# Performance work log

Measured on AMD Instinct MI355X. Metric: run time of the kernel, lower is better.

## Reference

```python
import jax, jax.numpy as jnp
import numpy as np

D_MODEL = 256; N_HEADS = 8; N_LEVELS = 4; N_POINTS = 4
D_HEAD = D_MODEL // N_HEADS


def setup_inputs() -> dict:
    key = jax.random.key(0)
    ks = jax.random.split(key, 8)
    N, Lq = 4, 4096
    shapes = np.array([4096, 2048, 1024, 512], dtype=np.int32)  # temporal lengths per level
    Len_in = int(shapes.sum())  # 7680
    start = np.concatenate([[0], np.cumsum(shapes)[:-1]]).astype(np.int32)
    HLP = N_HEADS * N_LEVELS * N_POINTS
    return {
        "query": jax.random.normal(ks[0], (N, Lq, D_MODEL), jnp.float32),
        "reference_points": jax.random.uniform(ks[1], (N, Lq, N_LEVELS, 1), jnp.float32),
        "input_flatten": jax.random.normal(ks[2], (N, Len_in, D_MODEL), jnp.float32),
        "input_spatial_shapes": jnp.asarray(shapes),
        "input_level_start_index": jnp.asarray(start),
        "W_off": jax.random.normal(ks[3], (D_MODEL, HLP), jnp.float32) * 0.01,
        "b_off": jax.random.normal(ks[4], (HLP,), jnp.float32) * 2.0,
        "W_aw": jax.random.normal(ks[5], (D_MODEL, HLP), jnp.float32) * 0.02,
        "b_aw": jnp.zeros((HLP,), jnp.float32),
        "W_v": jax.random.normal(ks[6], (D_MODEL, D_MODEL), jnp.float32) / np.sqrt(D_MODEL).astype(np.float32),
        "b_v": jnp.zeros((D_MODEL,), jnp.float32),
        "W_out": jax.random.normal(ks[7], (D_MODEL, D_MODEL), jnp.float32) / np.sqrt(D_MODEL).astype(np.float32),
        "b_out": jnp.zeros((D_MODEL,), jnp.float32),
    }


def reference(query, reference_points, input_flatten, input_spatial_shapes,
              input_level_start_index, W_off, b_off, W_aw, b_aw, W_v, b_v,
              W_out, b_out):
    N, Lq, C = query.shape
    M, L, P, Dh = N_HEADS, N_LEVELS, N_POINTS, D_HEAD
    S = input_flatten.shape[1]

    value = (input_flatten @ W_v + b_v).reshape(N, S, M, Dh)
    off = (query @ W_off + b_off).reshape(N, Lq, M, L, P)
    aw = jax.nn.softmax((query @ W_aw + b_aw).reshape(N, Lq, M, L * P), axis=-1)
    aw = aw.reshape(N, Lq, M, L, P)

    # reference_points last dim == 1 branch: loc = ref + off / T_l, in [0,1]
    T = input_spatial_shapes.astype(jnp.float32)[None, None, None, :, None]  # [1,1,1,L,1]
    loc = reference_points[:, :, None, :, None, 0] + off / T  # [N,Lq,M,L,P]

    # grid_sample(align_corners=False, padding_mode='border') along W with H=1, y=0.5:
    # pixel coord x = loc*T - 0.5, clamped to [0, T-1], then linear interp.
    x = jnp.clip(loc * T - 0.5, 0.0, T - 1.0)
    x0 = jnp.floor(x)
    w1 = x - x0                                   # frac weight for right neighbor
    i0 = x0.astype(jnp.int32)
    i1 = jnp.minimum(i0 + 1, input_spatial_shapes[None, None, None, :, None] - 1)
    base = input_level_start_index[None, None, None, :, None]
    g0 = i0 + base                                # global flattened indices [N,Lq,M,L,P]
    g1 = i1 + base

    v = value.transpose(0, 2, 1, 3)               # [N,M,S,Dh]

    def gather(idx):
        idxt = idx.transpose(0, 2, 1, 3, 4).reshape(N, M, Lq * L * P, 1)
        return jnp.take_along_axis(v, idxt, axis=2).reshape(N, M, Lq, L, P, Dh)

    s0 = gather(g0)
    s1 = gather(g1)
    w1t = w1.transpose(0, 2, 1, 3, 4)[..., None]   # [N,M,Lq,L,P,1]
    samp = s0 * (1.0 - w1t) + s1 * w1t             # [N,M,Lq,L,P,Dh]

    awt = aw.transpose(0, 2, 1, 3, 4)[..., None]
    out = (samp * awt).sum(axis=(3, 4))            # [N,M,Lq,Dh]
    out = out.transpose(0, 2, 1, 3).reshape(N, Lq, M * Dh)
    return out @ W_out + b_out
```

## Files before the change

kernel.cpp:

```cpp
#include <hip/hip_runtime.h>
#include <hip/hip_bf16.h>
#include <cstddef>
#include <cstdint>

#define D_MODEL   256
#define N_HEADS   8
#define N_LEVELS  4
#define N_POINTS  4
#define D_HEAD    32
#define HLP       128
#define NBATCH    4
#define LQ        4096
#define S_LEN     7680

typedef __attribute__((ext_vector_type(8))) short  short8;
typedef __attribute__((ext_vector_type(4))) float  f32x4;
typedef __attribute__((ext_vector_type(4))) int    i32x4;
typedef __attribute__((ext_vector_type(8))) unsigned short ushort8;

__device__ __forceinline__ unsigned short f2bf(float x) {
    __hip_bfloat16 h = __float2bfloat16(x);
    return *reinterpret_cast<unsigned short*>(&h);
}
__device__ __forceinline__ float bf2f(unsigned short u) {
    unsigned int v = ((unsigned int)u) << 16;
    return *reinterpret_cast<float*>(&v);
}

__device__ __forceinline__ void gload_lds16(const void* g, void* l) {
    __builtin_amdgcn_global_load_lds(
        (const __attribute__((address_space(1))) void*)g,
        (__attribute__((address_space(3))) void*)l,
        16, 0, 0);
}

__global__ __launch_bounds__(256) void prep_kernel(
    const float* __restrict__ W_v,  const float* __restrict__ W_off,
    const float* __restrict__ W_aw, const float* __restrict__ W_out,
    const float* __restrict__ b_off, const float* __restrict__ b_aw,
    unsigned short* __restrict__ Wv_t, unsigned short* __restrict__ Wcat_t,
    unsigned short* __restrict__ Wout_t, float* __restrict__ bcat)
{
    __shared__ float t[64][65];
    const int z   = blockIdx.z;
    const int k0  = blockIdx.y * 64;
    const int n0  = blockIdx.x * 64;
    const int tid = threadIdx.x;

    const float* src; int srcN; int cs; unsigned short* dst;
    if (z == 0)      { src = W_v;   srcN = 256; cs = n0;       dst = Wv_t;  }
    else if (z == 2) { src = W_out; srcN = 256; cs = n0;       dst = Wout_t;}
    else if (n0 < 128){ src = W_off; srcN = 128; cs = n0;      dst = Wcat_t;}
    else             { src = W_aw;  srcN = 128; cs = n0 - 128; dst = Wcat_t;}

    #pragma unroll
    for (int i = 0; i < 16; ++i) {
        int idx = tid + i * 256;
        int kk = idx >> 6, nn = idx & 63;
        t[kk][nn] = src[(size_t)(k0 + kk) * srcN + cs + nn];
    }
    __syncthreads();
    #pragma unroll
    for (int i = 0; i < 16; ++i) {
        int idx = tid + i * 256;
        int nn = idx >> 6, kk = idx & 63;
        dst[(size_t)(n0 + nn) * 256 + k0 + kk] = f2bf(t[kk][nn]);
    }
    if (z == 1 && blockIdx.x == 0 && blockIdx.y == 0) {
        bcat[tid] = (tid < 128) ? b_off[tid] : b_aw[tid - 128];
    }
}

__global__ __launch_bounds__(256) void gemm_vp_kernel(
    const float* __restrict__ inflat, const float* __restrict__ query,
    const unsigned short* __restrict__ Wv_t, const unsigned short* __restrict__ Wcat_t,
    const float* __restrict__ b_v, const float* __restrict__ bcat,
    unsigned short* __restrict__ value3, float* __restrict__ P)
{
    __shared__ alignas(16) unsigned short Abuf[2][4][64][8];
    __shared__ alignas(16) unsigned short Bbuf[2][8][64][8];

    const int job = blockIdx.x;
    const bool is_val = (job < 960);
    const int jj   = is_val ? job : (job - 960);
    const int row0 = (jj >> 1) * 64;
    const int col0 = (jj & 1) * 128;
    const float* A = is_val ? inflat : query;
    const unsigned short* Bt = is_val ? Wv_t : Wcat_t;
    const float* bias = is_val ? b_v : bcat;

    const int tid  = threadIdx.x;
    const int lane = tid & 63;
    const int w    = tid >> 6;
    const int lr   = lane & 15;
    const int lk   = (lane >> 4) * 8;

    const int ar = tid >> 2;
    const int ak = (tid & 3) * 8;
    const int afrag = ar >> 4;
    const int alane = ((ak >> 3) << 4) | (ar & 15);
    const float* Arow = A + (size_t)(row0 + ar) * 256 + ak;
    const unsigned short* Bcol = Bt + (size_t)(col0 + lr) * 256 + lk;

    f32x4 acc[8] = {};

    float4 pa0 = *(const float4*)(Arow);
    float4 pa1 = *(const float4*)(Arow + 4);
    #pragma unroll
    for (int c = 0; c < 2; ++c) {
        const int in = w * 2 + c;
        gload_lds16(Bcol + (size_t)in * 16 * 256, &Bbuf[0][in][0][0]);
    }

    for (int kt = 0; kt < 8; ++kt) {
        const int cur = kt & 1;
        short8 pk;
        pk[0] = (short)f2bf(pa0.x); pk[1] = (short)f2bf(pa0.y);
        pk[2] = (short)f2bf(pa0.z); pk[3] = (short)f2bf(pa0.w);
        pk[4] = (short)f2bf(pa1.x); pk[5] = (short)f2bf(pa1.y);
        pk[6] = (short)f2bf(pa1.z); pk[7] = (short)f2bf(pa1.w);
        *(short8*)&Abuf[cur][afrag][alane][0] = pk;
        __syncthreads();

        if (kt < 7) {
            const int k1 = (kt + 1) * 32;
            pa0 = *(const float4*)(Arow + k1);
            pa1 = *(const float4*)(Arow + k1 + 4);
            #pragma unroll
            for (int c = 0; c < 2; ++c) {
                const int in = w * 2 + c;
                gload_lds16(Bcol + (size_t)in * 16 * 256 + k1, &Bbuf[1 - cur][in][0][0]);
            }
        }

        const short8 af = *(const short8*)&Abuf[cur][w][lane][0];
        #pragma unroll
        for (int j = 0; j < 8; ++j) {
            const short8 bf = *(const short8*)&Bbuf[cur][j][lane][0];
            acc[j] = __builtin_amdgcn_mfma_f32_16x16x32_bf16(af, bf, acc[j], 0, 0, 0);
        }
    }

    const int prow = (lane >> 4) * 4;
    const int pcol = lane & 15;
    const int rbase = row0 + w * 16 + prow;
    if (is_val) {
        const int n  = row0 / S_LEN;
        const int s0 = row0 - n * S_LEN + w * 16 + prow;
        #pragma unroll
        for (int j = 0; j < 8; ++j) {
            const int col = col0 + j * 16 + pcol;
            const float bs = bias[col];
            const int m = col >> 5, d = col & 31;
            unsigned short* dst = value3 + ((size_t)(n * 8 + m) * S_LEN + s0) * 32 + d;
            #pragma unroll
            for (int r = 0; r < 4; ++r)
                dst[(size_t)r * 32] = f2bf(acc[j][r] + bs);
        }
    } else {
        #pragma unroll
        for (int j = 0; j < 8; ++j) {
            const int col = col0 + j * 16 + pcol;
            const float bs = bias[col];
            #pragma unroll
            for (int r = 0; r < 4; ++r)
                P[(size_t)(rbase + r) * 256 + col] = acc[j][r] + bs;
        }
    }
}

__global__ __launch_bounds__(512, 4) void sample_out_kernel(
    const float* __restrict__ P, const float* __restrict__ refp,
    const int* __restrict__ shapes, const int* __restrict__ lstart,
    const unsigned short* __restrict__ value3,
    const unsigned short* __restrict__ Wout_t,
    const float* __restrict__ b_out,
    float* __restrict__ Cout)
{
    __shared__ alignas(16) unsigned short t_lds[16][264];

    const int b    = blockIdx.x;
    const int xcd  = b & 7;
    const int n    = xcd >> 1;
    const int half = xcd & 1;
    const int slot = b >> 3;
    const int q0   = (slot * 2 + half) * 16;
    const int nq0  = n * LQ + q0;
    const int tid  = threadIdx.x;

    {
        const int q   = tid >> 5;
        const int sub = tid & 31;
        const int m   = sub >> 2;
        const int ql  = sub & 3;
        const int nq  = nq0 + q;

        const i32x4 sh4 = *(const i32x4*)shapes;
        const i32x4 ls4 = *(const i32x4*)lstart;
        const f32x4 rf4 = *(const f32x4*)(refp + (size_t)nq * N_LEVELS);

        float e[16], wgt[16];
        int   g0a[16], glim[4];
        #pragma unroll
        for (int l = 0; l < 4; ++l) {
            const f32x4 off = __builtin_nontemporal_load(
                (const f32x4*)(P + (size_t)nq * 256 + m * 16 + l * 4));
            const f32x4 lg  = __builtin_nontemporal_load(
                (const f32x4*)(P + (size_t)nq * 256 + 128 + m * 16 + l * 4));
            const float Tf = (float)sh4[l];
            glim[l] = ls4[l] + sh4[l] - 1;
            #pragma unroll
            for (int k = 0; k < 4; ++k) {
                float x = rf4[l] * Tf + off[k] - 0.5f;
                x = fminf(fmaxf(x, 0.0f), Tf - 1.0f);
                const float x0 = floorf(x);
                g0a[l * 4 + k] = (int)x0 + ls4[l];
                wgt[l * 4 + k] = x - x0;
                e  [l * 4 + k] = lg[k];
            }
        }

        float mx = -1e30f;
        #pragma unroll
        for (int i = 0; i < 16; ++i) mx = fmaxf(mx, e[i]);
        float s = 0.f;
        #pragma unroll
        for (int i = 0; i < 16; ++i) { e[i] = __expf(e[i] - mx); s += e[i]; }
        const float rs = 1.0f / s;

        const unsigned short* vb =
            value3 + (size_t)(n * 8 + m) * S_LEN * 32 + ql * 8;

        float acc[8] = {};
        #pragma unroll
        for (int i = 0; i < 16; ++i) {
            const float a  = e[i] * rs;
            const float ww = wgt[i];
            const int g0 = g0a[i];
            const int g1 = min(g0 + 1, glim[i >> 2]);
            const ushort8 u0 = *(const ushort8*)(vb + (size_t)g0 * 32);
            const ushort8 u1 = *(const ushort8*)(vb + (size_t)g1 * 32);
            #pragma unroll
            for (int d = 0; d < 8; ++d) {
                const float v0 = bf2f(u0[d]);
                const float v1 = bf2f(u1[d]);
                acc[d] += a * (v0 + ww * (v1 - v0));
            }
        }
        ushort8 o;
        #pragma unroll
        for (int d = 0; d < 8; ++d) o[d] = f2bf(acc[d]);
        *(ushort8*)&t_lds[q][m * 32 + ql * 8] = o;
    }
    __syncthreads();

    const int lane = tid & 63;
    const int wv   = tid >> 6;
    const int arow = lane & 15;
    const int kgrp = (lane >> 4) * 8;
    const int n0   = wv * 32;

    short8 af[8];
    #pragma unroll
    for (int kt = 0; kt < 8; ++kt)
        af[kt] = *(const short8*)&t_lds[arow][kt * 32 + kgrp];

    f32x4 oacc[2] = {};
    #pragma unroll
    for (int j = 0; j < 2; ++j) {
        const unsigned short* bp =
            Wout_t + (size_t)(n0 + j * 16 + arow) * 256 + kgrp;
        #pragma unroll
        for (int kt = 0; kt < 8; ++kt) {
            const short8 bf = *(const short8*)(bp + kt * 32);
            oacc[j] = __builtin_amdgcn_mfma_f32_16x16x32_bf16(af[kt], bf, oacc[j], 0, 0, 0);
        }
    }

    const int prow = (lane >> 4) * 4;
    const int pcol = lane & 15;
    #pragma unroll
    for (int j = 0; j < 2; ++j) {
        const int col = n0 + j * 16 + pcol;
        const float bs = b_out[col];
        #pragma unroll
        for (int r = 0; r < 4; ++r)
            __builtin_nontemporal_store(oacc[j][r] + bs,
                Cout + (size_t)(nq0 + prow + r) * 256 + col);
    }
}

extern "C" void kernel_launch(void* const* d_in, const int* in_sizes, int n_in,
                              void* d_out, int out_size, void* d_ws, size_t ws_size,
                              hipStream_t stream)
{
    const float* query  = (const float*)d_in[0];
    const float* refp   = (const float*)d_in[1];
    const float* inflat = (const float*)d_in[2];
    const int*   shapes = (const int*)d_in[3];
    const int*   lstart = (const int*)d_in[4];
    const float* W_off  = (const float*)d_in[5];
    const float* b_off  = (const float*)d_in[6];
    const float* W_aw   = (const float*)d_in[7];
    const float* b_aw   = (const float*)d_in[8];
    const float* W_v    = (const float*)d_in[9];
    const float* b_v    = (const float*)d_in[10];
    const float* W_out  = (const float*)d_in[11];
    const float* b_out  = (const float*)d_in[12];

    const int M_val = NBATCH * S_LEN;
    const int M_q   = NBATCH * LQ;

    char* p = (char*)d_ws;
    unsigned short* value3 = (unsigned short*)p; p += (size_t)M_val * D_MODEL * 2;
    float*          P      = (float*)p;          p += (size_t)M_q * 256 * 4;
    unsigned short* Wv_t   = (unsigned short*)p; p += 256 * 256 * 2;
    unsigned short* Wcat_t = (unsigned short*)p; p += 256 * 256 * 2;
    unsigned short* Wout_t = (unsigned short*)p; p += 256 * 256 * 2;
    float*          bcat   = (float*)p;          p += 256 * 4;

    prep_kernel<<<dim3(4, 4, 3), 256, 0, stream>>>(
        W_v, W_off, W_aw, W_out, b_off, b_aw, Wv_t, Wcat_t, Wout_t, bcat);
    gemm_vp_kernel<<<1472, 256, 0, stream>>>(
        inflat, query, Wv_t, Wcat_t, b_v, bcat, value3, P);
    sample_out_kernel<<<1024, 512, 0, stream>>>(
        P, refp, shapes, lstart, value3, Wout_t, b_out, (float*)d_out);
}
```

Measured before the change: 168.5 us.

## Split sampling levels across two lanes and halve queries per block

Each thread now samples only two of the four levels for its head slice, and partial sums from the paired lane are combined with a cross-lane shuffle. Blocks handle 8 queries instead of 16 and the grid is doubled, raising parallelism and in-flight gathers. The output GEMM still runs on 16 rows, half of them unused, so MFMA work and W_out loads per useful row double.

```diff
diff --git a/kernel.cpp b/kernel.cpp
--- a/kernel.cpp
+++ b/kernel.cpp
@@ -17,6 +17,7 @@
 typedef __attribute__((ext_vector_type(4))) float  f32x4;
 typedef __attribute__((ext_vector_type(4))) int    i32x4;
 typedef __attribute__((ext_vector_type(8))) unsigned short ushort8;
+typedef __attribute__((ext_vector_type(4))) unsigned short ushortv4;
 
 __device__ __forceinline__ unsigned short f2bf(float x) {
     __hip_bfloat16 h = __float2bfloat16(x);
@@ -184,39 +185,45 @@
     const int n    = xcd >> 1;
     const int half = xcd & 1;
     const int slot = b >> 3;
-    const int q0   = (slot * 2 + half) * 16;
+    const int q0   = (slot * 2 + half) * 8;
     const int nq0  = n * LQ + q0;
     const int tid  = threadIdx.x;
+    const int lane = tid & 63;
 
     {
-        const int q   = tid >> 5;
-        const int sub = tid & 31;
-        const int m   = sub >> 2;
-        const int ql  = sub & 3;
-        const int nq  = nq0 + q;
+        const int q  = tid >> 6;
+        const int m  = lane >> 3;
+        const int h  = (lane >> 2) & 1;
+        const int ql = lane & 3;
+        const int nq = nq0 + q;
 
         const i32x4 sh4 = *(const i32x4*)shapes;
         const i32x4 ls4 = *(const i32x4*)lstart;
         const f32x4 rf4 = *(const f32x4*)(refp + (size_t)nq * N_LEVELS);
 
-        float e[16], wgt[16];
-        int   g0a[16], glim[4];
+        float e[16];
         #pragma unroll
         for (int l = 0; l < 4; ++l) {
+            const f32x4 lg = __builtin_nontemporal_load(
+                (const f32x4*)(P + (size_t)nq * 256 + 128 + m * 16 + l * 4));
+            #pragma unroll
+            for (int k = 0; k < 4; ++k) e[l * 4 + k] = lg[k];
+        }
+        float wgt[8]; int g0a[8]; int glim2[2];
+        #pragma unroll
+        for (int li = 0; li < 2; ++li) {
+            const int l = h * 2 + li;
             const f32x4 off = __builtin_nontemporal_load(
                 (const f32x4*)(P + (size_t)nq * 256 + m * 16 + l * 4));
-            const f32x4 lg  = __builtin_nontemporal_load(
-                (const f32x4*)(P + (size_t)nq * 256 + 128 + m * 16 + l * 4));
             const float Tf = (float)sh4[l];
-            glim[l] = ls4[l] + sh4[l] - 1;
+            glim2[li] = ls4[l] + sh4[l] - 1;
             #pragma unroll
             for (int k = 0; k < 4; ++k) {
                 float x = rf4[l] * Tf + off[k] - 0.5f;
                 x = fminf(fmaxf(x, 0.0f), Tf - 1.0f);
                 const float x0 = floorf(x);
-                g0a[l * 4 + k] = (int)x0 + ls4[l];
-                wgt[l * 4 + k] = x - x0;
-                e  [l * 4 + k] = lg[k];
+                g0a[li * 4 + k] = (int)x0 + ls4[l];
+                wgt[li * 4 + k] = x - x0;
             }
         }
 
@@ -233,11 +240,11 @@
 
         float acc[8] = {};
         #pragma unroll
-        for (int i = 0; i < 16; ++i) {
-            const float a  = e[i] * rs;
+        for (int i = 0; i < 8; ++i) {
+            const float a  = e[h * 8 + i] * rs;
             const float ww = wgt[i];
             const int g0 = g0a[i];
-            const int g1 = min(g0 + 1, glim[i >> 2]);
+            const int g1 = min(g0 + 1, glim2[i >> 2]);
             const ushort8 u0 = *(const ushort8*)(vb + (size_t)g0 * 32);
             const ushort8 u1 = *(const ushort8*)(vb + (size_t)g1 * 32);
             #pragma unroll
@@ -247,14 +254,16 @@
                 acc[d] += a * (v0 + ww * (v1 - v0));
             }
         }
-        ushort8 o;
-        #pragma unroll
-        for (int d = 0; d < 8; ++d) o[d] = f2bf(acc[d]);
-        *(ushort8*)&t_lds[q][m * 32 + ql * 8] = o;
+        #pragma unroll
+        for (int d = 0; d < 8; ++d) acc[d] += __shfl_xor(acc[d], 4);
+
+        ushortv4 o4;
+        #pragma unroll
+        for (int d = 0; d < 4; ++d) o4[d] = f2bf(acc[h * 4 + d]);
+        *(ushortv4*)&t_lds[q][m * 32 + ql * 8 + h * 4] = o4;
     }
     __syncthreads();
 
-    const int lane = tid & 63;
     const int wv   = tid >> 6;
     const int arow = lane & 15;
     const int kgrp = (lane >> 4) * 8;
@@ -279,14 +288,16 @@
 
     const int prow = (lane >> 4) * 4;
     const int pcol = lane & 15;
-    #pragma unroll
-    for (int j = 0; j < 2; ++j) {
-        const int col = n0 + j * 16 + pcol;
-        const float bs = b_out[col];
-        #pragma unroll
-        for (int r = 0; r < 4; ++r)
-            __builtin_nontemporal_store(oacc[j][r] + bs,
-                Cout + (size_t)(nq0 + prow + r) * 256 + col);
+    if (prow < 8) {
+        #pragma unroll
+        for (int j = 0; j < 2; ++j) {
+            const int col = n0 + j * 16 + pcol;
+            const float bs = b_out[col];
+            #pragma unroll
+            for (int r = 0; r < 4; ++r)
+                __builtin_nontemporal_store(oacc[j][r] + bs,
+                    Cout + (size_t)(nq0 + prow + r) * 256 + col);
+        }
     }
 }
 
@@ -323,6 +334,6 @@
         W_v, W_off, W_aw, W_out, b_off, b_aw, Wv_t, Wcat_t, Wout_t, bcat);
     gemm_vp_kernel<<<1472, 256, 0, stream>>>(
         inflat, query, Wv_t, Wcat_t, b_v, bcat, value3, P);
-    sample_out_kernel<<<1024, 512, 0, stream>>>(
+    sample_out_kernel<<<2048, 512, 0, stream>>>(
         P, refp, shapes, lstart, value3, Wout_t, b_out, (float*)d_out);
 }
```

Measured after the change: 182.7 us. 1.08x slower.

## Fuse query offset/attention projection into sampling kernel, drop P buffer

Applied to the files above, without the earlier changes.

The query projection (offsets and attention logits) is removed from the value GEMM kernel and computed inside the sampling kernel. Each block converts its 16 query rows to bf16, runs an MFMA GEMM against the concatenated weights, and keeps the results in a shared-memory buffer. This removes the fp32 P intermediate's global write and read and shrinks the first GEMM launch. The cost is extra shared memory and a GEMM phase at the start of every sampling block, which may reduce occupancy and lengthen that kernel.

```diff
diff --git a/kernel.cpp b/kernel.cpp
--- a/kernel.cpp
+++ b/kernel.cpp
@@ -71,23 +71,18 @@
     }
 }
 
-__global__ __launch_bounds__(256) void gemm_vp_kernel(
-    const float* __restrict__ inflat, const float* __restrict__ query,
-    const unsigned short* __restrict__ Wv_t, const unsigned short* __restrict__ Wcat_t,
-    const float* __restrict__ b_v, const float* __restrict__ bcat,
-    unsigned short* __restrict__ value3, float* __restrict__ P)
+__global__ __launch_bounds__(256) void gemm_v_kernel(
+    const float* __restrict__ inflat,
+    const unsigned short* __restrict__ Wv_t,
+    const float* __restrict__ b_v,
+    unsigned short* __restrict__ value3)
 {
     __shared__ alignas(16) unsigned short Abuf[2][4][64][8];
     __shared__ alignas(16) unsigned short Bbuf[2][8][64][8];
 
-    const int job = blockIdx.x;
-    const bool is_val = (job < 960);
-    const int jj   = is_val ? job : (job - 960);
+    const int jj   = blockIdx.x;
     const int row0 = (jj >> 1) * 64;
     const int col0 = (jj & 1) * 128;
-    const float* A = is_val ? inflat : query;
-    const unsigned short* Bt = is_val ? Wv_t : Wcat_t;
-    const float* bias = is_val ? b_v : bcat;
 
     const int tid  = threadIdx.x;
     const int lane = tid & 63;
@@ -99,8 +94,8 @@
     const int ak = (tid & 3) * 8;
     const int afrag = ar >> 4;
     const int alane = ((ak >> 3) << 4) | (ar & 15);
-    const float* Arow = A + (size_t)(row0 + ar) * 256 + ak;
-    const unsigned short* Bcol = Bt + (size_t)(col0 + lr) * 256 + lk;
+    const float* Arow = inflat + (size_t)(row0 + ar) * 256 + ak;
+    const unsigned short* Bcol = Wv_t + (size_t)(col0 + lr) * 256 + lk;
 
     f32x4 acc[8] = {};
 
@@ -143,41 +138,32 @@
 
     const int prow = (lane >> 4) * 4;
     const int pcol = lane & 15;
-    const int rbase = row0 + w * 16 + prow;
-    if (is_val) {
-        const int n  = row0 / S_LEN;
-        const int s0 = row0 - n * S_LEN + w * 16 + prow;
-        #pragma unroll
-        for (int j = 0; j < 8; ++j) {
-            const int col = col0 + j * 16 + pcol;
-            const float bs = bias[col];
-            const int m = col >> 5, d = col & 31;
-            unsigned short* dst = value3 + ((size_t)(n * 8 + m) * S_LEN + s0) * 32 + d;
-            #pragma unroll
-            for (int r = 0; r < 4; ++r)
-                dst[(size_t)r * 32] = f2bf(acc[j][r] + bs);
-        }
-    } else {
-        #pragma unroll
-        for (int j = 0; j < 8; ++j) {
-            const int col = col0 + j * 16 + pcol;
-            const float bs = bias[col];
-            #pragma unroll
-            for (int r = 0; r < 4; ++r)
-                P[(size_t)(rbase + r) * 256 + col] = acc[j][r] + bs;
-        }
+    const int n  = row0 / S_LEN;
+    const int s0 = row0 - n * S_LEN + w * 16 + prow;
+    #pragma unroll
+    for (int j = 0; j < 8; ++j) {
+        const int col = col0 + j * 16 + pcol;
+        const float bs = b_v[col];
+        const int m = col >> 5, d = col & 31;
+        unsigned short* dst = value3 + ((size_t)(n * 8 + m) * S_LEN + s0) * 32 + d;
+        #pragma unroll
+        for (int r = 0; r < 4; ++r)
+            dst[(size_t)r * 32] = f2bf(acc[j][r] + bs);
     }
 }
 
 __global__ __launch_bounds__(512, 4) void sample_out_kernel(
-    const float* __restrict__ P, const float* __restrict__ refp,
+    const float* __restrict__ query, const float* __restrict__ refp,
     const int* __restrict__ shapes, const int* __restrict__ lstart,
     const unsigned short* __restrict__ value3,
+    const unsigned short* __restrict__ Wcat_t,
+    const float* __restrict__ bcat,
     const unsigned short* __restrict__ Wout_t,
     const float* __restrict__ b_out,
     float* __restrict__ Cout)
 {
     __shared__ alignas(16) unsigned short t_lds[16][264];
+    __shared__ alignas(16) float pbuf[16][264];
 
     const int b    = blockIdx.x;
     const int xcd  = b & 7;
@@ -187,6 +173,57 @@
     const int q0   = (slot * 2 + half) * 16;
     const int nq0  = n * LQ + q0;
     const int tid  = threadIdx.x;
+    const int lane = tid & 63;
+    const int wv   = tid >> 6;
+
+    {
+        const int row = tid >> 5;
+        const int c0  = (tid & 31) * 8;
+        const float* qp = query + (size_t)(nq0 + row) * 256 + c0;
+        const float4 a  = *(const float4*)qp;
+        const float4 b4 = *(const float4*)(qp + 4);
+        short8 pk;
+        pk[0] = (short)f2bf(a.x);  pk[1] = (short)f2bf(a.y);
+        pk[2] = (short)f2bf(a.z);  pk[3] = (short)f2bf(a.w);
+        pk[4] = (short)f2bf(b4.x); pk[5] = (short)f2bf(b4.y);
+        pk[6] = (short)f2bf(b4.z); pk[7] = (short)f2bf(b4.w);
+        *(short8*)&t_lds[row][c0] = pk;
+    }
+    __syncthreads();
+
+    {
+        const int arow = lane & 15;
+        const int kgrp = (lane >> 4) * 8;
+        const int n0   = wv * 32;
+
+        short8 af[8];
+        #pragma unroll
+        for (int kt = 0; kt < 8; ++kt)
+            af[kt] = *(const short8*)&t_lds[arow][kt * 32 + kgrp];
+
+        f32x4 pacc[2] = {};
+        #pragma unroll
+        for (int j = 0; j < 2; ++j) {
+            const unsigned short* bp =
+                Wcat_t + (size_t)(n0 + j * 16 + arow) * 256 + kgrp;
+            #pragma unroll
+            for (int kt = 0; kt < 8; ++kt) {
+                const short8 bf = *(const short8*)(bp + kt * 32);
+                pacc[j] = __builtin_amdgcn_mfma_f32_16x16x32_bf16(af[kt], bf, pacc[j], 0, 0, 0);
+            }
+        }
+        const int prow = (lane >> 4) * 4;
+        const int pcol = lane & 15;
+        #pragma unroll
+        for (int j = 0; j < 2; ++j) {
+            const int col = n0 + j * 16 + pcol;
+            const float bs = bcat[col];
+            #pragma unroll
+            for (int r = 0; r < 4; ++r)
+                pbuf[prow + r][col] = pacc[j][r] + bs;
+        }
+    }
+    __syncthreads();
 
     {
         const int q   = tid >> 5;
@@ -203,10 +240,8 @@
         int   g0a[16], glim[4];
         #pragma unroll
         for (int l = 0; l < 4; ++l) {
-            const f32x4 off = __builtin_nontemporal_load(
-                (const f32x4*)(P + (size_t)nq * 256 + m * 16 + l * 4));
-            const f32x4 lg  = __builtin_nontemporal_load(
-                (const f32x4*)(P + (size_t)nq * 256 + 128 + m * 16 + l * 4));
+            const f32x4 off = *(const f32x4*)&pbuf[q][m * 16 + l * 4];
+            const f32x4 lg  = *(const f32x4*)&pbuf[q][128 + m * 16 + l * 4];
             const float Tf = (float)sh4[l];
             glim[l] = ls4[l] + sh4[l] - 1;
             #pragma unroll
@@ -254,39 +289,39 @@
     }
     __syncthreads();
 
-    const int lane = tid & 63;
-    const int wv   = tid >> 6;
-    const int arow = lane & 15;
-    const int kgrp = (lane >> 4) * 8;
-    const int n0   = wv * 32;
-
-    short8 af[8];
-    #pragma unroll
-    for (int kt = 0; kt < 8; ++kt)
-        af[kt] = *(const short8*)&t_lds[arow][kt * 32 + kgrp];
-
-    f32x4 oacc[2] = {};
-    #pragma unroll
-    for (int j = 0; j < 2; ++j) {
-        const unsigned short* bp =
-            Wout_t + (size_t)(n0 + j * 16 + arow) * 256 + kgrp;
-        #pragma unroll
-        for (int kt = 0; kt < 8; ++kt) {
-            const short8 bf = *(const short8*)(bp + kt * 32);
-            oacc[j] = __builtin_amdgcn_mfma_f32_16x16x32_bf16(af[kt], bf, oacc[j], 0, 0, 0);
-        }
-    }
-
-    const int prow = (lane >> 4) * 4;
-    const int pcol = lane & 15;
-    #pragma unroll
-    for (int j = 0; j < 2; ++j) {
-        const int col = n0 + j * 16 + pcol;
-        const float bs = b_out[col];
-        #pragma unroll
-        for (int r = 0; r < 4; ++r)
-            __builtin_nontemporal_store(oacc[j][r] + bs,
-                Cout + (size_t)(nq0 + prow + r) * 256 + col);
+    {
+        const int arow = lane & 15;
+        const int kgrp = (lane >> 4) * 8;
+        const int n0   = wv * 32;
+
+        short8 af[8];
+        #pragma unroll
+        for (int kt = 0; kt < 8; ++kt)
+            af[kt] = *(const short8*)&t_lds[arow][kt * 32 + kgrp];
+
+        f32x4 oacc[2] = {};
+        #pragma unroll
+        for (int j = 0; j < 2; ++j) {
+            const unsigned short* bp =
+                Wout_t + (size_t)(n0 + j * 16 + arow) * 256 + kgrp;
+            #pragma unroll
+            for (int kt = 0; kt < 8; ++kt) {
+                const short8 bf = *(const short8*)(bp + kt * 32);
+                oacc[j] = __builtin_amdgcn_mfma_f32_16x16x32_bf16(af[kt], bf, oacc[j], 0, 0, 0);
+            }
+        }
+
+        const int prow = (lane >> 4) * 4;
+        const int pcol = lane & 15;
+        #pragma unroll
+        for (int j = 0; j < 2; ++j) {
+            const int col = n0 + j * 16 + pcol;
+            const float bs = b_out[col];
+            #pragma unroll
+            for (int r = 0; r < 4; ++r)
+                __builtin_nontemporal_store(oacc[j][r] + bs,
+                    Cout + (size_t)(nq0 + prow + r) * 256 + col);
+        }
     }
 }
 
@@ -309,11 +344,9 @@
     const float* b_out  = (const float*)d_in[12];
 
     const int M_val = NBATCH * S_LEN;
-    const int M_q   = NBATCH * LQ;
 
     char* p = (char*)d_ws;
     unsigned short* value3 = (unsigned short*)p; p += (size_t)M_val * D_MODEL * 2;
-    float*          P      = (float*)p;          p += (size_t)M_q * 256 * 4;
     unsigned short* Wv_t   = (unsigned short*)p; p += 256 * 256 * 2;
     unsigned short* Wcat_t = (unsigned short*)p; p += 256 * 256 * 2;
     unsigned short* Wout_t = (unsigned short*)p; p += 256 * 256 * 2;
@@ -321,8 +354,9 @@
 
     prep_kernel<<<dim3(4, 4, 3), 256, 0, stream>>>(
         W_v, W_off, W_aw, W_out, b_off, b_aw, Wv_t, Wcat_t, Wout_t, bcat);
-    gemm_vp_kernel<<<1472, 256, 0, stream>>>(
-        inflat, query, Wv_t, Wcat_t, b_v, bcat, value3, P);
+    gemm_v_kernel<<<960, 256, 0, stream>>>(
+        inflat, Wv_t, b_v, value3);
     sample_out_kernel<<<1024, 512, 0, stream>>>(
-        P, refp, shapes, lstart, value3, Wout_t, b_out, (float*)d_out);
-}
+        query, refp, shapes, lstart, value3, Wcat_t, bcat,
+        Wout_t, b_out, (float*)d_out);
+}
```

Result: no change. 169.4 us (+0.5%).
